# Kernel optimization log

Hardware: AMD Instinct MI355X
Metric: run time of the kernel (lower is better)

## Reference

```python
import jax, jax.numpy as jnp
import numpy as np

N_IDX = 4
N_LATENT = 6
D_IDX = 2 ** N_IDX
D_LATENT = 2 ** N_LATENT
D = D_IDX * D_LATENT  # 1024
TIME_EMBED = 128
BATCH = 32


def _build_H():
    # S_plus |k> = |(k+1) mod d_idx>, H_idx = S_plus + S_plus^T, H = H_idx kron I_latent
    S_plus = np.zeros((D_IDX, D_IDX), dtype=np.float32)
    for k in range(D_IDX):
        S_plus[(k + 1) % D_IDX, k] = 1.0
    H_idx = S_plus + S_plus.T
    H = np.kron(H_idx, np.eye(D_LATENT, dtype=np.float32))
    return jnp.asarray(H)


def setup_inputs() -> dict:
    key = jax.random.key(0)
    k_rho, k_t, k_w1, k_b1, k_w2, k_b2 = jax.random.split(key, 6)
    # PSD density-like rho so the trace normalization is well-conditioned
    A = jax.random.normal(k_rho, (BATCH, D, D), dtype=jnp.float32)
    rho = jnp.einsum('bij,bkj->bik', A, A) / D
    t = jax.random.uniform(k_t, (BATCH,), dtype=jnp.float32)
    # lambda_net: Linear(1, E) -> SiLU -> Linear(E, 1) -> Tanh (torch Linear: weight (out,in))
    w1 = jax.random.normal(k_w1, (TIME_EMBED, 1), dtype=jnp.float32) * 1.0
    b1 = jax.random.uniform(k_b1, (TIME_EMBED,), dtype=jnp.float32, minval=-1.0, maxval=1.0)
    w2 = jax.random.normal(k_w2, (1, TIME_EMBED), dtype=jnp.float32) * (1.0 / np.sqrt(TIME_EMBED))
    b2 = jax.random.uniform(k_b2, (1,), dtype=jnp.float32, minval=-0.09, maxval=0.09)
    H = _build_H()
    return {'rho': rho, 't': t, 'w1': w1, 'b1': b1, 'w2': w2, 'b2': b2, 'H': H}


def reference(rho, t, w1, b1, w2, b2, H):
    # lambda(t) = 0.1 * tanh(Linear(SiLU(Linear(t))))
    x = t[:, None]  # (B, 1)
    h = jax.nn.silu(x @ w1.T + b1)  # (B, E)
    lam = jnp.tanh(h @ w2.T + b2)[:, 0] * 0.1  # (B,)
    # Shared eigendecomposition of constant symmetric H
    eigvals, eigvecs = jnp.linalg.eigh(H)  # (D,), (D, D)
    exp_diag = jnp.exp(-lam[:, None] * eigvals[None, :])  # (B, D)
    # U_b = V diag(exp_diag_b) V^T, batched
    U = jnp.einsum('id,bd,jd->bij', eigvecs, exp_diag, eigvecs)  # (B, D, D)
    rho_out = jnp.einsum('bij,bjk,blk->bil', U, rho, U)  # U rho U^T
    trace = jnp.trace(rho_out, axis1=-2, axis2=-1)[:, None, None]
    return rho_out / jnp.maximum(trace, 1e-8)
```

## Files before the change

kernel.cpp:

```cpp
#include <hip/hip_runtime.h>

#define DI 16
#define DL 64
#define DD 1024
#define NB 32
#define TE 128
#define PI_F 3.14159265358979323846f

#define WS_E   0
#define WS_G   (NB*256)
#define WS_TRP (2*NB*256)

__global__ void k_prep(const float* __restrict__ t,
                       const float* __restrict__ w1,
                       const float* __restrict__ b1,
                       const float* __restrict__ w2,
                       const float* __restrict__ b2,
                       float* __restrict__ ws) {
    int b = blockIdx.x;
    int tid = threadIdx.x;

    __shared__ float red[2];
    __shared__ float lam_sh;
    __shared__ float ck[16];
    __shared__ float ek[16], e2k[16];

    float tb = t[b];
    float z = tb * w1[tid] + b1[tid];
    float h = z / (1.0f + expf(-z));
    float v = h * w2[tid];
    #pragma unroll
    for (int off = 32; off; off >>= 1) v += __shfl_down(v, off, 64);
    if ((tid & 63) == 0) red[tid >> 6] = v;
    __syncthreads();
    if (tid == 0) {
        float y = red[0] + red[1] + b2[0];
        lam_sh = tanhf(y) * 0.1f;
    }
    if (tid < 16) ck[tid] = cosf((PI_F / 8.0f) * (float)tid);
    __syncthreads();
    float lam = lam_sh;
    if (tid < 16) {
        ek[tid]  = expf(-2.0f * lam * ck[tid]);
        e2k[tid] = expf(-4.0f * lam * ck[tid]);
    }
    __syncthreads();
    for (int idx = tid; idx < 256; idx += 128) {
        int i = idx >> 4, j = idx & 15;
        int r = (i - j) & 15;
        float se = 0.0f, sg = 0.0f;
        #pragma unroll
        for (int k = 0; k < 16; k++) {
            float c = ck[(k * r) & 15];
            se += ek[k] * c;
            sg += e2k[k] * c;
        }
        ws[WS_E + b * 256 + idx] = se * (1.0f / 16.0f);
        ws[WS_G + b * 256 + idx] = sg * (1.0f / 16.0f);
    }
}

__global__ void k_trace(const float* __restrict__ rho, float* __restrict__ ws) {
    int c = blockIdx.x;
    int b = blockIdx.y;
    int tid = threadIdx.x;
    __shared__ float Gs[16];
    __shared__ float part[4];

    if (tid < 16) Gs[tid] = ws[WS_G + b * 256 + c * 16 + tid];
    __syncthreads();

    int p  = tid & 63;
    int dg = tid >> 6;
    const float* rowp = rho + (size_t)b * DD * DD + (size_t)(c * 64 + p) * DD + p;
    float s = 0.0f;
    #pragma unroll
    for (int i = 0; i < 4; i++) {
        int d = dg * 4 + i;
        s += Gs[d] * rowp[d * 64];
    }
    #pragma unroll
    for (int off = 32; off; off >>= 1) s += __shfl_down(s, off, 64);
    if ((tid & 63) == 0) part[tid >> 6] = s;
    __syncthreads();
    if (tid == 0)
        ws[WS_TRP + b * 16 + c] = part[0] + part[1] + part[2] + part[3];
}

__global__ __launch_bounds__(256, 2)
void k_main(const float* __restrict__ rho, const float* __restrict__ ws,
            float* __restrict__ out) {
    __shared__ float S[16 * 512];
    __shared__ float T[16 * 516];
    __shared__ float Es[256];
    __shared__ float sinv_sh;

    int qt  = blockIdx.x;
    int p   = blockIdx.y;
    int b   = blockIdx.z;
    int tid = threadIdx.x;
    int q0  = qt * 32;

    if (tid < 64)
        ((float4*)Es)[tid] = ((const float4*)(ws + WS_E + b * 256))[tid];
    if (tid == 0) {
        float tr = 0.0f;
        #pragma unroll
        for (int c = 0; c < 16; c++) tr += ws[WS_TRP + b * 16 + c];
        sinv_sh = 1.0f / fmaxf(tr, 1e-8f);
    }

    const float* rbase = rho + (size_t)b * (DD * DD) + q0;
    #pragma unroll
    for (int it = 0; it < 8; it++) {
        int g  = it * 256 + tid;
        int c  = g >> 7;
        int r  = g & 127;
        int d  = r >> 3;
        int q4 = r & 7;
        float4 v = *(const float4*)(rbase + (size_t)(c * 64 + p) * DD + d * 64 + q4 * 4);
        *(float4*)&S[c * 512 + d * 32 + q4 * 4] = v;
    }
    __syncthreads();

    {
        int ah = tid >> 7;
        int d  = (tid >> 3) & 15;
        int qq = (tid & 7) * 4;
        float4 acc[8];
        #pragma unroll
        for (int i = 0; i < 8; i++) acc[i] = make_float4(0.f, 0.f, 0.f, 0.f);
        #pragma unroll
        for (int c = 0; c < 16; c++) {
            float4 s4 = *(float4*)&S[c * 512 + d * 32 + qq];
            float4 e0 = *(float4*)&Es[c * 16 + ah * 8];
            float4 e1 = *(float4*)&Es[c * 16 + ah * 8 + 4];
            acc[0].x += e0.x * s4.x; acc[0].y += e0.x * s4.y; acc[0].z += e0.x * s4.z; acc[0].w += e0.x * s4.w;
            acc[1].x += e0.y * s4.x; acc[1].y += e0.y * s4.y; acc[1].z += e0.y * s4.z; acc[1].w += e0.y * s4.w;
            acc[2].x += e0.z * s4.x; acc[2].y += e0.z * s4.y; acc[2].z += e0.z * s4.z; acc[2].w += e0.z * s4.w;
            acc[3].x += e0.w * s4.x; acc[3].y += e0.w * s4.y; acc[3].z += e0.w * s4.z; acc[3].w += e0.w * s4.w;
            acc[4].x += e1.x * s4.x; acc[4].y += e1.x * s4.y; acc[4].z += e1.x * s4.z; acc[4].w += e1.x * s4.w;
            acc[5].x += e1.y * s4.x; acc[5].y += e1.y * s4.y; acc[5].z += e1.y * s4.z; acc[5].w += e1.y * s4.w;
            acc[6].x += e1.z * s4.x; acc[6].y += e1.z * s4.y; acc[6].z += e1.z * s4.z; acc[6].w += e1.z * s4.w;
            acc[7].x += e1.w * s4.x; acc[7].y += e1.w * s4.y; acc[7].z += e1.w * s4.z; acc[7].w += e1.w * s4.w;
        }
        #pragma unroll
        for (int ai = 0; ai < 8; ai++)
            *(float4*)&T[(ah * 8 + ai) * 516 + d * 32 + qq] = acc[ai];
    }
    __syncthreads();

    {
        int ah = tid >> 7;
        int bp = (tid >> 3) & 15;
        int qq = (tid & 7) * 4;
        float Eb[16];
        #pragma unroll
        for (int j4 = 0; j4 < 4; j4++) {
            float4 e = *(float4*)&Es[bp * 16 + j4 * 4];
            Eb[4 * j4 + 0] = e.x; Eb[4 * j4 + 1] = e.y; Eb[4 * j4 + 2] = e.z; Eb[4 * j4 + 3] = e.w;
        }
        float sinv = sinv_sh;
        float* obase = out + (size_t)b * (DD * DD) + (size_t)p * DD + bp * 64 + q0 + qq;
        #pragma unroll
        for (int ai = 0; ai < 8; ai++) {
            int a = ah * 8 + ai;
            float4 acc = make_float4(0.f, 0.f, 0.f, 0.f);
            #pragma unroll
            for (int d = 0; d < 16; d++) {
                float4 t4 = *(float4*)&T[a * 516 + d * 32 + qq];
                acc.x += Eb[d] * t4.x; acc.y += Eb[d] * t4.y;
                acc.z += Eb[d] * t4.z; acc.w += Eb[d] * t4.w;
            }
            acc.x *= sinv; acc.y *= sinv; acc.z *= sinv; acc.w *= sinv;
            *(float4*)(obase + (size_t)a * (64 * DD)) = acc;
        }
    }
}

extern "C" void kernel_launch(void* const* d_in, const int* in_sizes, int n_in,
                              void* d_out, int out_size, void* d_ws, size_t ws_size,
                              hipStream_t stream) {
    const float* rho = (const float*)d_in[0];
    const float* t   = (const float*)d_in[1];
    const float* w1  = (const float*)d_in[2];
    const float* b1  = (const float*)d_in[3];
    const float* w2  = (const float*)d_in[4];
    const float* b2  = (const float*)d_in[5];
    float* out = (float*)d_out;
    float* ws  = (float*)d_ws;

    k_prep <<<NB, 128, 0, stream>>>(t, w1, b1, w2, b2, ws);
    k_trace<<<dim3(DI, NB), 256, 0, stream>>>(rho, ws);
    k_main <<<dim3(2, 64, NB), 256, 0, stream>>>(rho, ws, out);
}
```

Baseline: 70.39 us.

## Fold prep kernel into trace and main kernels, use direct global-to-LDS loads

```diff
diff --git a/kernel.cpp b/kernel.cpp
--- a/kernel.cpp
+++ b/kernel.cpp
@@ -1,73 +1,53 @@
 #include <hip/hip_runtime.h>
+#include <stdint.h>
 
 #define DI 16
 #define DL 64
 #define DD 1024
 #define NB 32
-#define TE 128
 #define PI_F 3.14159265358979323846f
 
-#define WS_E   0
-#define WS_G   (NB*256)
-#define WS_TRP (2*NB*256)
-
-__global__ void k_prep(const float* __restrict__ t,
-                       const float* __restrict__ w1,
-                       const float* __restrict__ b1,
-                       const float* __restrict__ w2,
-                       const float* __restrict__ b2,
-                       float* __restrict__ ws) {
-    int b = blockIdx.x;
-    int tid = threadIdx.x;
-
-    __shared__ float red[2];
-    __shared__ float lam_sh;
-    __shared__ float ck[16];
-    __shared__ float ek[16], e2k[16];
-
-    float tb = t[b];
-    float z = tb * w1[tid] + b1[tid];
-    float h = z / (1.0f + expf(-z));
-    float v = h * w2[tid];
-    #pragma unroll
-    for (int off = 32; off; off >>= 1) v += __shfl_down(v, off, 64);
-    if ((tid & 63) == 0) red[tid >> 6] = v;
-    __syncthreads();
-    if (tid == 0) {
-        float y = red[0] + red[1] + b2[0];
-        lam_sh = tanhf(y) * 0.1f;
-    }
-    if (tid < 16) ck[tid] = cosf((PI_F / 8.0f) * (float)tid);
-    __syncthreads();
-    float lam = lam_sh;
-    if (tid < 16) {
-        ek[tid]  = expf(-2.0f * lam * ck[tid]);
-        e2k[tid] = expf(-4.0f * lam * ck[tid]);
-    }
-    __syncthreads();
-    for (int idx = tid; idx < 256; idx += 128) {
-        int i = idx >> 4, j = idx & 15;
-        int r = (i - j) & 15;
-        float se = 0.0f, sg = 0.0f;
-        #pragma unroll
-        for (int k = 0; k < 16; k++) {
-            float c = ck[(k * r) & 15];
-            se += ek[k] * c;
-            sg += e2k[k] * c;
-        }
-        ws[WS_E + b * 256 + idx] = se * (1.0f / 16.0f);
-        ws[WS_G + b * 256 + idx] = sg * (1.0f / 16.0f);
-    }
-}
-
-__global__ void k_trace(const float* __restrict__ rho, float* __restrict__ ws) {
+#define AS1 __attribute__((address_space(1)))
+#define AS3 __attribute__((address_space(3)))
+
+
+__global__ void k_trace(const float* __restrict__ rho,
+                        const float* __restrict__ t,
+                        const float* __restrict__ w1,
+                        const float* __restrict__ b1,
+                        const float* __restrict__ w2,
+                        const float* __restrict__ b2,
+                        float* __restrict__ ws) {
     int c = blockIdx.x;
     int b = blockIdx.y;
     int tid = threadIdx.x;
+    __shared__ float lam_sh;
+    __shared__ float ck[16];
     __shared__ float Gs[16];
     __shared__ float part[4];
 
-    if (tid < 16) Gs[tid] = ws[WS_G + b * 256 + c * 16 + tid];
+    if (tid < 64) {
+        float tb = t[b];
+        float z0 = tb * w1[tid]      + b1[tid];
+        float z1 = tb * w1[tid + 64] + b1[tid + 64];
+        float h0 = z0 / (1.0f + expf(-z0));
+        float h1 = z1 / (1.0f + expf(-z1));
+        float v = h0 * w2[tid] + h1 * w2[tid + 64];
+        #pragma unroll
+        for (int off = 32; off; off >>= 1) v += __shfl_down(v, off, 64);
+        if (tid == 0) lam_sh = tanhf(v + b2[0]) * 0.1f;
+    }
+    if (tid >= 64 && tid < 80) ck[tid - 64] = cosf((PI_F / 8.0f) * (float)(tid - 64));
+    __syncthreads();
+    if (tid < 16) {
+        float lam = lam_sh;
+        int r = (c - tid) & 15;
+        float sg = 0.0f;
+        #pragma unroll
+        for (int k = 0; k < 16; k++)
+            sg += expf(-4.0f * lam * ck[k]) * ck[(k * r) & 15];
+        Gs[tid] = sg * (1.0f / 16.0f);
+    }
     __syncthreads();
 
     int p  = tid & 63;
@@ -84,31 +64,29 @@
     if ((tid & 63) == 0) part[tid >> 6] = s;
     __syncthreads();
     if (tid == 0)
-        ws[WS_TRP + b * 16 + c] = part[0] + part[1] + part[2] + part[3];
+        ws[b * 16 + c] = part[0] + part[1] + part[2] + part[3];
 }
 
 __global__ __launch_bounds__(256, 2)
-void k_main(const float* __restrict__ rho, const float* __restrict__ ws,
+void k_main(const float* __restrict__ rho,
+            const float* __restrict__ t,
+            const float* __restrict__ w1,
+            const float* __restrict__ b1,
+            const float* __restrict__ w2,
+            const float* __restrict__ b2,
+            const float* __restrict__ ws,
             float* __restrict__ out) {
     __shared__ float S[16 * 512];
     __shared__ float T[16 * 516];
     __shared__ float Es[256];
-    __shared__ float sinv_sh;
+    __shared__ float ck[16];
+    __shared__ float lam_sh, sinv_sh;
 
     int qt  = blockIdx.x;
     int p   = blockIdx.y;
     int b   = blockIdx.z;
     int tid = threadIdx.x;
     int q0  = qt * 32;
-
-    if (tid < 64)
-        ((float4*)Es)[tid] = ((const float4*)(ws + WS_E + b * 256))[tid];
-    if (tid == 0) {
-        float tr = 0.0f;
-        #pragma unroll
-        for (int c = 0; c < 16; c++) tr += ws[WS_TRP + b * 16 + c];
-        sinv_sh = 1.0f / fmaxf(tr, 1e-8f);
-    }
 
     const float* rbase = rho + (size_t)b * (DD * DD) + q0;
     #pragma unroll
@@ -118,8 +96,41 @@
         int r  = g & 127;
         int d  = r >> 3;
         int q4 = r & 7;
-        float4 v = *(const float4*)(rbase + (size_t)(c * 64 + p) * DD + d * 64 + q4 * 4);
-        *(float4*)&S[c * 512 + d * 32 + q4 * 4] = v;
+        const float* ga = rbase + (size_t)(c * 64 + p) * DD + d * 64 + q4 * 4;
+        int gw = it * 256 + (tid & ~63);
+        unsigned fo = (unsigned)((gw >> 7) * 512 + (gw & 127) * 4);
+        __builtin_amdgcn_global_load_lds((const AS1 uint32_t*)ga,
+                                         (AS3 uint32_t*)&S[fo], 16, 0, 0);
+    }
+
+    if (tid < 64) {
+        float tb = t[b];
+        float z0 = tb * w1[tid]      + b1[tid];
+        float z1 = tb * w1[tid + 64] + b1[tid + 64];
+        float h0 = z0 / (1.0f + expf(-z0));
+        float h1 = z1 / (1.0f + expf(-z1));
+        float v = h0 * w2[tid] + h1 * w2[tid + 64];
+        #pragma unroll
+        for (int off = 32; off; off >>= 1) v += __shfl_down(v, off, 64);
+        if (tid == 0) lam_sh = tanhf(v + b2[0]) * 0.1f;
+    }
+    if (tid >= 64 && tid < 80) ck[tid - 64] = cosf((PI_F / 8.0f) * (float)(tid - 64));
+    if (tid == 128) {
+        float tr = 0.0f;
+        #pragma unroll
+        for (int c = 0; c < 16; c++) tr += ws[b * 16 + c];
+        sinv_sh = 1.0f / fmaxf(tr, 1e-8f);
+    }
+    __syncthreads();
+
+    {
+        float lam = lam_sh;
+        int i = tid >> 4, j = tid & 15, r = (i - j) & 15;
+        float se = 0.0f;
+        #pragma unroll
+        for (int k = 0; k < 16; k++)
+            se += expf(-2.0f * lam * ck[k]) * ck[(k * r) & 15];
+        Es[tid] = se * (1.0f / 16.0f);
     }
     __syncthreads();
 
@@ -190,7 +201,6 @@
     float* out = (float*)d_out;
     float* ws  = (float*)d_ws;
 
-    k_prep <<<NB, 128, 0, stream>>>(t, w1, b1, w2, b2, ws);
-    k_trace<<<dim3(DI, NB), 256, 0, stream>>>(rho, ws);
-    k_main <<<dim3(2, 64, NB), 256, 0, stream>>>(rho, ws, out);
+    k_trace<<<dim3(DI, NB), 256, 0, stream>>>(rho, t, w1, b1, w2, b2, ws);
+    k_main <<<dim3(2, 64, NB), 256, 0, stream>>>(rho, t, w1, b1, w2, b2, ws, out);
 }
```

New measurement: 73.57 us. 1.05x slower.
